# Optimization experiments

Hardware: AMD Instinct MI355X
Metric: run time of the kernel (lower is better)

The kernel has to match this reference:

```python
import jax, jax.numpy as jnp
import numpy as np

C_CURV = 0.01
EPS = 1e-10


def _log_map_zero(x, c):
    sc = jnp.sqrt(c)
    n = jnp.maximum(jnp.linalg.norm(x, axis=-1, keepdims=True), EPS)
    arg = jnp.minimum(sc * n, 1.0 - 1e-7)  # keep arctanh finite
    return jnp.arctanh(arg) * x / (sc * n)


def _exp_map_zero(v, c):
    sc = jnp.sqrt(c)
    n = jnp.maximum(jnp.linalg.norm(v, axis=-1, keepdims=True), EPS)
    return jnp.tanh(sc * n) * v / (sc * n)


def setup_inputs() -> dict:
    key = jax.random.key(0)
    k1, k2, k3, k4, k5, k6 = jax.random.split(key, 6)
    num_entities, d, R = 50000, 1024, 2000
    B = 32768
    # entity embeddings live on the Poincare ball: keep sqrt(c)*||x|| << 1
    entity_embedding = 0.01 * jax.random.normal(k1, (num_entities, d), dtype=jnp.float32)
    rel_embedding = 0.02 * jax.random.normal(k2, (R, d), dtype=jnp.float32)  # tangent space
    triplets = jax.random.randint(k3, (B, 3), 0, num_entities, dtype=jnp.int64)
    lim = float(np.sqrt(6.0 / (d + d)))  # xavier_uniform
    W_s = jax.random.uniform(k4, (d, d), dtype=jnp.float32, minval=-lim, maxval=lim)
    W_o = jax.random.uniform(k5, (d, d), dtype=jnp.float32, minval=-lim, maxval=lim)
    rel_bias = jnp.zeros((R,), dtype=jnp.float32)
    return {"entity_embedding": entity_embedding, "rel_embedding": rel_embedding,
            "triplets": triplets, "W_s": W_s, "W_o": W_o, "rel_bias": rel_bias}


def reference(entity_embedding, rel_embedding, triplets, W_s, W_o, rel_bias):
    c = C_CURV
    s_emb = entity_embedding[triplets[:, 0]]  # (B, d)
    o_emb = entity_embedding[triplets[:, 2]]
    s_tan = _log_map_zero(s_emb, c)
    o_tan = _log_map_zero(o_emb, c)
    query_tan = s_tan @ W_s + o_tan @ W_o  # dropout p=0 -> identity
    query = _exp_map_zero(query_tan, c)    # (B, d)
    rel_hyp = _exp_map_zero(rel_embedding, c)  # (R, d)
    # diff = mobius_add(-q, r, c); dist_sq = ||diff||^2, computed in closed form
    # from ||x||^2, ||y||^2, <x, y> with x = -q, y = r (no B*R*d expansion).
    xx = jnp.sum(query * query, axis=-1)        # (B,)  ||-q||^2 == ||q||^2
    yy = jnp.sum(rel_hyp * rel_hyp, axis=-1)    # (R,)
    xy = -(query @ rel_hyp.T)                   # (B, R)  <-q, r>
    A = 1.0 + 2.0 * c * xy + c * yy[None, :]
    Bc = 1.0 - c * xx[:, None]
    num_sq = A * A * xx[:, None] + 2.0 * A * Bc * xy + Bc * Bc * yy[None, :]
    den = 1.0 + 2.0 * c * xy + (c * c) * xx[:, None] * yy[None, :]
    dist_sq = num_sq / (den * den)
    return -dist_sq + rel_bias[None, :]  # (B, R)
```

## Files before the change

### kernel.cpp

```cpp
#include <hip/hip_runtime.h>
#include <hip/hip_bf16.h>

typedef __attribute__((ext_vector_type(4))) int i32x4;

#define CC 0.01f
#define SCRT 0.1f

#define SA 1814.2857f
#define SW 2343.1734f
#define SQf 1270.0f
#define SR 1104.3478f
#define Q1 (1.0f / (SA * SW))
#define Q2 (1.0f / (SQf * SR))

static __device__ __forceinline__ unsigned char f2i8(float x, float S) {
  float v = fminf(fmaxf(x * S, -127.0f), 127.0f);
  return (unsigned char)(signed char)__float2int_rn(v);
}

#define GLOAD16(g, l) __builtin_amdgcn_global_load_lds( \
    (const __attribute__((address_space(1))) void*)(g), \
    (__attribute__((address_space(3))) void*)(l), 16, 0, 0)

__global__ void k_prep_sto(const float* __restrict__ ent,
                           const int* __restrict__ trip,
                           unsigned char* __restrict__ sto8) {
  int i = blockIdx.x;
  int t = threadIdx.x;
  size_t si = (size_t)trip[i * 3 + 0];
  size_t oi = (size_t)trip[i * 3 + 2];
  float4 vs = ((const float4*)(ent + si * 1024))[t];
  float4 vo = ((const float4*)(ent + oi * 1024))[t];
  float ss = vs.x * vs.x + vs.y * vs.y + vs.z * vs.z + vs.w * vs.w;
  float so = vo.x * vo.x + vo.y * vo.y + vo.z * vo.z + vo.w * vo.w;
#pragma unroll
  for (int off = 32; off > 0; off >>= 1) {
    ss += __shfl_down(ss, off, 64);
    so += __shfl_down(so, off, 64);
  }
  __shared__ float red[8];
  if ((t & 63) == 0) { red[t >> 6] = ss; red[4 + (t >> 6)] = so; }
  __syncthreads();
  float tot_s = red[0] + red[1] + red[2] + red[3];
  float tot_o = red[4] + red[5] + red[6] + red[7];

  float ns = fmaxf(sqrtf(tot_s), 1e-10f);
  float scn_s = SCRT * ns;
  float fs = atanhf(fminf(scn_s, 1.0f - 1e-7f)) / scn_s;
  float no = fmaxf(sqrtf(tot_o), 1e-10f);
  float scn_o = SCRT * no;
  float fo = atanhf(fminf(scn_o, 1.0f - 1e-7f)) / scn_o;

  uchar4 os, oo;
  os.x = f2i8(vs.x * fs, SA); os.y = f2i8(vs.y * fs, SA);
  os.z = f2i8(vs.z * fs, SA); os.w = f2i8(vs.w * fs, SA);
  oo.x = f2i8(vo.x * fo, SA); oo.y = f2i8(vo.y * fo, SA);
  oo.z = f2i8(vo.z * fo, SA); oo.w = f2i8(vo.w * fo, SA);
  ((uchar4*)(sto8 + (size_t)i * 2048))[t] = os;
  ((uchar4*)(sto8 + (size_t)i * 2048 + 1024))[t] = oo;
}

__global__ void k_wt(const float* __restrict__ Ws, const float* __restrict__ Wo,
                     unsigned char* __restrict__ wt8) {
  int idx = blockIdx.x * 256 + threadIdx.x;
  int n = idx >> 11;
  int k = idx & 2047;
  float v = (k < 1024) ? Ws[k * 1024 + n] : Wo[(k - 1024) * 1024 + n];
  wt8[idx] = f2i8(v, SW);
}

__global__ void k_rel(const float* __restrict__ rel,
                      unsigned char* __restrict__ relb8,
                      float* __restrict__ yy, float* __restrict__ fj) {
  int j = blockIdx.x;
  int t = threadIdx.x;
  float4 v = ((const float4*)(rel + (size_t)j * 1024))[t];
  float ss = v.x * v.x + v.y * v.y + v.z * v.z + v.w * v.w;
#pragma unroll
  for (int off = 32; off > 0; off >>= 1) ss += __shfl_down(ss, off, 64);
  __shared__ float red[4];
  if ((t & 63) == 0) red[t >> 6] = ss;
  __syncthreads();
  uchar4 o;
  o.x = f2i8(v.x, SR); o.y = f2i8(v.y, SR);
  o.z = f2i8(v.z, SR); o.w = f2i8(v.w, SR);
  ((uchar4*)(relb8 + (size_t)j * 1024))[t] = o;
  if (t == 0) {
    float tot = red[0] + red[1] + red[2] + red[3];
    float n = fmaxf(sqrtf(tot), 1e-10f);
    float scn = SCRT * n;
    float f = tanhf(scn) / scn;
    yy[j] = f * f * tot;
    fj[j] = f;
  }
}

__global__ void k_qstat(const unsigned char* __restrict__ qt8,
                        float* __restrict__ xx, float* __restrict__ fi) {
  int i = blockIdx.x;
  int t = threadIdx.x;
  uchar4 v = ((const uchar4*)(qt8 + (size_t)i * 1024))[t];
  int a = (signed char)v.x, b = (signed char)v.y;
  int c = (signed char)v.z, d = (signed char)v.w;
  int ss = a * a + b * b + c * c + d * d;
#pragma unroll
  for (int off = 32; off > 0; off >>= 1) ss += __shfl_down(ss, off, 64);
  __shared__ int red[4];
  if ((t & 63) == 0) red[t >> 6] = ss;
  __syncthreads();
  if (t == 0) {
    float tot = (float)(red[0] + red[1] + red[2] + red[3]) * (1.0f / (SQf * SQf));
    float n = fmaxf(sqrtf(tot), 1e-10f);
    float scn = SCRT * n;
    float f = tanhf(scn) / scn;
    xx[i] = f * f * tot;
    fi[i] = f;
  }
}

template<int K, bool G2>
__global__ __launch_bounds__(256, 4) void k_gemm_i8(
    const unsigned char* __restrict__ A8,
    const unsigned char* __restrict__ B8,
    unsigned char* __restrict__ qt8out,
    const float* __restrict__ xx, const float* __restrict__ fi,
    const float* __restrict__ yy, const float* __restrict__ fj,
    const float* __restrict__ bias, float* __restrict__ out,
    int nxb) {
  constexpr int NT = K / 64;
  __shared__ __align__(16) unsigned char AS[2 * 8192];
  __shared__ __align__(16) unsigned char BS[2 * 8192];

  int nwg = gridDim.x;
  int bid = blockIdx.x;
  int wg = (bid & 7) * (nwg >> 3) + (bid >> 3);
  int bx = wg % nxb;
  int by = wg / nxb;
  size_t gm0 = (size_t)by * 128;
  int gn0 = bx * 128;

  int t = threadIdx.x;
  int lane = t & 63;
  int w = t >> 6;
  int wr = w >> 1;
  int wc = w & 1;
  int fr = lane & 15;
  int k0l = lane >> 4;

  int r1 = t >> 2;
  int ch = (t & 3) ^ ((r1 >> 1) & 3);
  const unsigned char* pa0 = A8 + (gm0 + r1) * (size_t)K + ch * 16;
  const unsigned char* pa1 = pa0 + (size_t)64 * K;
  int br0 = gn0 + r1, br1 = gn0 + 64 + r1;
  if (G2) { br0 = min(br0, 1999); br1 = min(br1, 1999); }
  const unsigned char* pb0 = B8 + (size_t)br0 * K + ch * 16;
  const unsigned char* pb1 = B8 + (size_t)br1 * K + ch * 16;

  char* aw = (char*)AS + w * 1024;
  char* bw = (char*)BS + w * 1024;

  unsigned fca = (unsigned)((k0l ^ ((fr >> 1) & 3)) << 4);
  const char* ard = (const char*)AS + (wr * 64 + fr) * 64 + fca;
  const char* brd = (const char*)BS + (wc * 64 + fr) * 64 + fca;

#define STAGE(kt, slot) do { \
    size_t ko_ = (size_t)(kt) * 64; \
    GLOAD16(pa0 + ko_, aw + (slot) * 8192); \
    GLOAD16(pa1 + ko_, aw + (slot) * 8192 + 4096); \
    GLOAD16(pb0 + ko_, bw + (slot) * 8192); \
    GLOAD16(pb1 + ko_, bw + (slot) * 8192 + 4096); \
  } while (0)

  i32x4 acc[4][4] = {};

  STAGE(0, 0);

  for (int kt = 0; kt < NT; ++kt) {
    __syncthreads();
    if (kt + 1 < NT) STAGE(kt + 1, (kt + 1) & 1);
    int slot = (kt & 1) * 8192;
    i32x4 af[4], bf[4];
#pragma unroll
    for (int m = 0; m < 4; ++m) af[m] = *(const i32x4*)(ard + slot + m * 1024);
#pragma unroll
    for (int n = 0; n < 4; ++n) bf[n] = *(const i32x4*)(brd + slot + n * 1024);
#pragma unroll
    for (int m = 0; m < 4; ++m)
#pragma unroll
      for (int n = 0; n < 4; ++n)
        acc[m][n] = __builtin_amdgcn_mfma_i32_16x16x64_i8(af[m], bf[n], acc[m][n], 0, 0, 0);
  }
#undef STAGE

  if (!G2) {
#pragma unroll
    for (int m = 0; m < 4; ++m)
#pragma unroll
      for (int n = 0; n < 4; ++n) {
        int col = gn0 + wc * 64 + n * 16 + fr;
        size_t row0 = gm0 + wr * 64 + m * 16 + k0l * 4;
#pragma unroll
        for (int j = 0; j < 4; ++j) {
          float v = (float)acc[m][n][j] * Q1;
          qt8out[(row0 + j) * 1024 + col] = f2i8(v, SQf);
        }
      }
  } else {
#pragma unroll
    for (int m = 0; m < 4; ++m)
#pragma unroll
      for (int n = 0; n < 4; ++n) {
        int col = gn0 + wc * 64 + n * 16 + fr;
        if (col < 2000) {
          float yj = yy[col], fjc = fj[col], bj = bias[col];
          size_t row0 = gm0 + wr * 64 + m * 16 + k0l * 4;
#pragma unroll
          for (int j = 0; j < 4; ++j) {
            size_t row = row0 + j;
            float G = (float)acc[m][n][j] * Q2;
            float xi = xx[row], fic = fi[row];
            float xyv = -(fic * fjc) * G;
            float Aa = 1.0f + 2.0f * CC * xyv + CC * yj;
            float Bb = 1.0f - CC * xi;
            float num = Aa * Aa * xi + 2.0f * Aa * Bb * xyv + Bb * Bb * yj;
            float den = 1.0f + 2.0f * CC * xyv + CC * CC * xi * yj;
            out[row * 2000 + col] = -(num / (den * den)) + bj;
          }
        }
      }
  }
}

extern "C" void kernel_launch(void* const* d_in, const int* in_sizes, int n_in,
                              void* d_out, int out_size, void* d_ws, size_t ws_size,
                              hipStream_t stream) {
  const float* ent = (const float*)d_in[0];
  const float* rel = (const float*)d_in[1];
  const int* trip = (const int*)d_in[2];
  const float* Ws = (const float*)d_in[3];
  const float* Wo = (const float*)d_in[4];
  const float* bias = (const float*)d_in[5];
  float* out = (float*)d_out;

  char* ws = (char*)d_ws;
  unsigned char* sto8  = (unsigned char*)(ws);
  unsigned char* qt8   = (unsigned char*)(ws + 67108864);
  unsigned char* wt8   = (unsigned char*)(ws + 100663296);
  unsigned char* relb8 = (unsigned char*)(ws + 102760448);
  float* xx = (float*)(ws + 104857600);
  float* fi = (float*)(ws + 104988672);
  float* yy = (float*)(ws + 105119744);
  float* fj = (float*)(ws + 105127936);

  k_prep_sto<<<dim3(32768), dim3(256), 0, stream>>>(ent, trip, sto8);
  k_wt<<<dim3((1024 * 2048) / 256), dim3(256), 0, stream>>>(Ws, Wo, wt8);
  k_rel<<<dim3(2000), dim3(256), 0, stream>>>(rel, relb8, yy, fj);

  k_gemm_i8<2048, false><<<dim3(2048), dim3(256), 0, stream>>>(
      sto8, wt8, qt8, xx, fi, yy, fj, bias, out, 8);

  k_qstat<<<dim3(32768), dim3(256), 0, stream>>>(qt8, xx, fi);

  k_gemm_i8<1024, true><<<dim3(4096), dim3(256), 0, stream>>>(
      qt8, relb8, qt8 , xx, fi, yy, fj, bias, out, 16);
}
```

Measured before the change: 324.6 us.

## Fuse query norm into GEMM1 epilogue, tile weight transpose, simplify distance epilogue

The separate k_qstat pass, which reread the int8 query matrix, is removed. The first GEMM's epilogue now computes per-row sums of squares with wave shuffles and atomicAdds them into a zeroed buffer, and a small k_fi kernel turns those sums into the tanh factors. The weight transpose/quantize kernel now goes through an LDS tile with coalesced float4 reads. The second GEMM's epilogue hoists per-row terms out of the inner loop and replaces the divide with a hardware reciprocal. Risks: the norm now comes from the unquantized values rather than the int8 ones, atomics make the result order-nondeterministic, and the fast reciprocal is less precise.

After: 328.1 us. About the same (+1.1%).

```diff
diff --git a/kernel.cpp b/kernel.cpp
--- a/kernel.cpp
+++ b/kernel.cpp
@@ -21,6 +21,10 @@
 #define GLOAD16(g, l) __builtin_amdgcn_global_load_lds( \
     (const __attribute__((address_space(1))) void*)(g), \
     (__attribute__((address_space(3))) void*)(l), 16, 0, 0)
+
+__global__ void k_zero(float* __restrict__ p) {
+  p[blockIdx.x * 256 + threadIdx.x] = 0.0f;
+}
 
 __global__ void k_prep_sto(const float* __restrict__ ent,
                            const int* __restrict__ trip,
@@ -60,13 +64,40 @@
   ((uchar4*)(sto8 + (size_t)i * 2048 + 1024))[t] = oo;
 }
 
-__global__ void k_wt(const float* __restrict__ Ws, const float* __restrict__ Wo,
-                     unsigned char* __restrict__ wt8) {
-  int idx = blockIdx.x * 256 + threadIdx.x;
-  int n = idx >> 11;
-  int k = idx & 2047;
-  float v = (k < 1024) ? Ws[k * 1024 + n] : Wo[(k - 1024) * 1024 + n];
-  wt8[idx] = f2i8(v, SW);
+__global__ void k_wt_t(const float* __restrict__ Ws,
+                       const float* __restrict__ Wo,
+                       unsigned char* __restrict__ wt8) {
+  __shared__ float lds[64][65];
+  int bid = blockIdx.x;
+  int mat = bid >> 8;
+  int rem = bid & 255;
+  int k0 = (rem >> 4) * 64;
+  int n0 = (rem & 15) * 64;
+  const float* src = mat ? Wo : Ws;
+  int t = threadIdx.x;
+  int kk = t >> 4;
+  int nq = t & 15;
+#pragma unroll
+  for (int r = 0; r < 4; ++r) {
+    int k = r * 16 + kk;
+    float4 v = *(const float4*)(src + (size_t)(k0 + k) * 1024 + n0 + nq * 4);
+    lds[k][nq * 4 + 0] = v.x;
+    lds[k][nq * 4 + 1] = v.y;
+    lds[k][nq * 4 + 2] = v.z;
+    lds[k][nq * 4 + 3] = v.w;
+  }
+  __syncthreads();
+  int kq = t & 15;
+#pragma unroll
+  for (int q = 0; q < 4; ++q) {
+    int nn = q * 16 + (t >> 4);
+    uchar4 o;
+    o.x = f2i8(lds[kq * 4 + 0][nn], SW);
+    o.y = f2i8(lds[kq * 4 + 1][nn], SW);
+    o.z = f2i8(lds[kq * 4 + 2][nn], SW);
+    o.w = f2i8(lds[kq * 4 + 3][nn], SW);
+    *(uchar4*)(wt8 + (size_t)(n0 + nn) * 2048 + mat * 1024 + k0 + kq * 4) = o;
+  }
 }
 
 __global__ void k_rel(const float* __restrict__ rel,
@@ -95,27 +126,15 @@
   }
 }
 
-__global__ void k_qstat(const unsigned char* __restrict__ qt8,
-                        float* __restrict__ xx, float* __restrict__ fi) {
-  int i = blockIdx.x;
-  int t = threadIdx.x;
-  uchar4 v = ((const uchar4*)(qt8 + (size_t)i * 1024))[t];
-  int a = (signed char)v.x, b = (signed char)v.y;
-  int c = (signed char)v.z, d = (signed char)v.w;
-  int ss = a * a + b * b + c * c + d * d;
-#pragma unroll
-  for (int off = 32; off > 0; off >>= 1) ss += __shfl_down(ss, off, 64);
-  __shared__ int red[4];
-  if ((t & 63) == 0) red[t >> 6] = ss;
-  __syncthreads();
-  if (t == 0) {
-    float tot = (float)(red[0] + red[1] + red[2] + red[3]) * (1.0f / (SQf * SQf));
-    float n = fmaxf(sqrtf(tot), 1e-10f);
-    float scn = SCRT * n;
-    float f = tanhf(scn) / scn;
-    xx[i] = f * f * tot;
-    fi[i] = f;
-  }
+__global__ void k_fi(const float* __restrict__ xxacc,
+                     float* __restrict__ xx, float* __restrict__ fi) {
+  int i = blockIdx.x * 256 + threadIdx.x;
+  float tot = xxacc[i];
+  float n = fmaxf(sqrtf(tot), 1e-10f);
+  float scn = SCRT * n;
+  float f = tanhf(scn) / scn;
+  xx[i] = f * f * tot;
+  fi[i] = f;
 }
 
 template<int K, bool G2>
@@ -123,6 +142,7 @@
     const unsigned char* __restrict__ A8,
     const unsigned char* __restrict__ B8,
     unsigned char* __restrict__ qt8out,
+    float* __restrict__ xxacc,
     const float* __restrict__ xx, const float* __restrict__ fi,
     const float* __restrict__ yy, const float* __restrict__ fj,
     const float* __restrict__ bias, float* __restrict__ out,
@@ -194,40 +214,71 @@
 
   if (!G2) {
 #pragma unroll
-    for (int m = 0; m < 4; ++m)
+    for (int m = 0; m < 4; ++m) {
+      size_t row0 = gm0 + wr * 64 + m * 16 + k0l * 4;
+      float rs0 = 0.0f, rs1 = 0.0f, rs2 = 0.0f, rs3 = 0.0f;
 #pragma unroll
       for (int n = 0; n < 4; ++n) {
         int col = gn0 + wc * 64 + n * 16 + fr;
-        size_t row0 = gm0 + wr * 64 + m * 16 + k0l * 4;
-#pragma unroll
-        for (int j = 0; j < 4; ++j) {
-          float v = (float)acc[m][n][j] * Q1;
-          qt8out[(row0 + j) * 1024 + col] = f2i8(v, SQf);
-        }
+        float v0 = (float)acc[m][n][0] * Q1;
+        float v1 = (float)acc[m][n][1] * Q1;
+        float v2 = (float)acc[m][n][2] * Q1;
+        float v3 = (float)acc[m][n][3] * Q1;
+        rs0 = fmaf(v0, v0, rs0); rs1 = fmaf(v1, v1, rs1);
+        rs2 = fmaf(v2, v2, rs2); rs3 = fmaf(v3, v3, rs3);
+        qt8out[(row0 + 0) * 1024 + col] = f2i8(v0, SQf);
+        qt8out[(row0 + 1) * 1024 + col] = f2i8(v1, SQf);
+        qt8out[(row0 + 2) * 1024 + col] = f2i8(v2, SQf);
+        qt8out[(row0 + 3) * 1024 + col] = f2i8(v3, SQf);
       }
+      float rs[4] = {rs0, rs1, rs2, rs3};
+#pragma unroll
+      for (int j = 0; j < 4; ++j) {
+        float s = rs[j];
+        s += __shfl_xor(s, 1, 64);
+        s += __shfl_xor(s, 2, 64);
+        s += __shfl_xor(s, 4, 64);
+        s += __shfl_xor(s, 8, 64);
+        if (fr == 0) atomicAdd(&xxacc[row0 + j], s);
+      }
+    }
   } else {
 #pragma unroll
-    for (int m = 0; m < 4; ++m)
+    for (int m = 0; m < 4; ++m) {
+      size_t row0 = gm0 + wr * 64 + m * 16 + k0l * 4;
+      float xi_[4], fic_[4], Bb_[4], u2_[4], b2_[4];
+#pragma unroll
+      for (int j = 0; j < 4; ++j) {
+        xi_[j] = xx[row0 + j];
+        fic_[j] = fi[row0 + j];
+        Bb_[j] = 1.0f - CC * xi_[j];
+        u2_[j] = Bb_[j] + Bb_[j];
+        b2_[j] = Bb_[j] * Bb_[j];
+      }
 #pragma unroll
       for (int n = 0; n < 4; ++n) {
         int col = gn0 + wc * 64 + n * 16 + fr;
         if (col < 2000) {
           float yj = yy[col], fjc = fj[col], bj = bias[col];
-          size_t row0 = gm0 + wr * 64 + m * 16 + k0l * 4;
+          float ycc = fmaf(CC, yj, 1.0f);
+          float cyj = CC * yj;
+          float b2yj0 = b2_[0] * yj, b2yj1 = b2_[1] * yj;
+          float b2yj2 = b2_[2] * yj, b2yj3 = b2_[3] * yj;
+          float b2yj_[4] = {b2yj0, b2yj1, b2yj2, b2yj3};
 #pragma unroll
           for (int j = 0; j < 4; ++j) {
-            size_t row = row0 + j;
             float G = (float)acc[m][n][j] * Q2;
-            float xi = xx[row], fic = fi[row];
-            float xyv = -(fic * fjc) * G;
-            float Aa = 1.0f + 2.0f * CC * xyv + CC * yj;
-            float Bb = 1.0f - CC * xi;
-            float num = Aa * Aa * xi + 2.0f * Aa * Bb * xyv + Bb * Bb * yj;
-            float den = 1.0f + 2.0f * CC * xyv + CC * CC * xi * yj;
-            out[row * 2000 + col] = -(num / (den * den)) + bj;
+            float xyv = -(fic_[j] * fjc) * G;
+            float Aa = fmaf(2.0f * CC, xyv, ycc);
+            float den = fmaf(-cyj, Bb_[j], Aa);
+            float tt = fmaf(u2_[j], xyv, Aa * xi_[j]);
+            float num = fmaf(Aa, tt, b2yj_[j]);
+            float r = __builtin_amdgcn_rcpf(den);
+            out[(row0 + j) * 2000 + col] = fmaf(-num, r * r, bj);
           }
         }
       }
+    }
   }
 }
 
@@ -247,20 +298,22 @@
   unsigned char* qt8   = (unsigned char*)(ws + 67108864);
   unsigned char* wt8   = (unsigned char*)(ws + 100663296);
   unsigned char* relb8 = (unsigned char*)(ws + 102760448);
-  float* xx = (float*)(ws + 104857600);
-  float* fi = (float*)(ws + 104988672);
-  float* yy = (float*)(ws + 105119744);
-  float* fj = (float*)(ws + 105127936);
-
+  float* xx    = (float*)(ws + 104857600);
+  float* fi    = (float*)(ws + 104988672);
+  float* yy    = (float*)(ws + 105119744);
+  float* fj    = (float*)(ws + 105127936);
+  float* xxacc = (float*)(ws + 105136128);
+
+  k_zero<<<dim3(128), dim3(256), 0, stream>>>(xxacc);
   k_prep_sto<<<dim3(32768), dim3(256), 0, stream>>>(ent, trip, sto8);
-  k_wt<<<dim3((1024 * 2048) / 256), dim3(256), 0, stream>>>(Ws, Wo, wt8);
+  k_wt_t<<<dim3(512), dim3(256), 0, stream>>>(Ws, Wo, wt8);
   k_rel<<<dim3(2000), dim3(256), 0, stream>>>(rel, relb8, yy, fj);
 
   k_gemm_i8<2048, false><<<dim3(2048), dim3(256), 0, stream>>>(
-      sto8, wt8, qt8, xx, fi, yy, fj, bias, out, 8);
-
-  k_qstat<<<dim3(32768), dim3(256), 0, stream>>>(qt8, xx, fi);
+      sto8, wt8, qt8, xxacc, xx, fi, yy, fj, bias, out, 8);
+
+  k_fi<<<dim3(128), dim3(256), 0, stream>>>(xxacc, xx, fi);
 
   k_gemm_i8<1024, true><<<dim3(4096), dim3(256), 0, stream>>>(
-      qt8, relb8, qt8 , xx, fi, yy, fj, bias, out, 16);
-}
+      qt8, relb8, qt8 , xxacc, xx, fi, yy, fj, bias, out, 16);
+}
```
